# Performance work log

Hardware: AMD Instinct MI355X
Metric: run time of the kernel (lower is better)

The kernel has to match this reference:

```python
import jax, jax.numpy as jnp
import numpy as np

N_FEAT = 32
P = 3            # patch_size
K = 4            # top-k
DS = (3, 5, 7)   # displacement windows for (l3, l2, l1)
T = 3            # n_frames
EPS = 1e-12      # F.normalize eps


def _unfold(x, ksz):
    # F.unfold(x, ksz, padding=ksz//2, stride=1): [b,c,h,w] -> [b,c,ksz*ksz,h,w]
    b, c, h, w = x.shape
    pad = ksz // 2
    xp = jnp.pad(x, ((0, 0), (0, 0), (pad, pad), (pad, pad)))
    pats = [xp[:, :, i:i + h, j:j + w] for i in range(ksz) for j in range(ksz)]
    return jnp.stack(pats, axis=2)


def _agg_unit(feat_t, feat_tm1, d, agg_w, agg_b, wp_w, wp_b):
    b, c, h, w = feat_t.shape
    p2 = P * P
    ft_u = _unfold(feat_t, P).reshape(b, c * p2, h, w)        # [b,cp2,h,w]
    ftm_u = _unfold(feat_tm1, P).reshape(b, c * p2, h, w)     # [b,cp2,h,w]
    disp = jnp.transpose(_unfold(ftm_u, d), (0, 1, 3, 4, 2))  # [b,cp2,h,w,d2]
    # cosine similarity over channel*patch dim
    ft_n = ft_u / jnp.maximum(jnp.linalg.norm(ft_u, axis=1, keepdims=True), EPS)
    disp_norm = jnp.maximum(jnp.linalg.norm(disp, axis=1), EPS)          # [b,h,w,d2]
    sim = jnp.einsum('bchw,bchwd->bhwd', ft_n, disp) / disp_norm          # [b,h,w,d2]
    _, idx = jax.lax.top_k(sim, K)                                        # [b,h,w,K]
    gath = jnp.take_along_axis(disp, idx[:, None], axis=-1)               # [b,cp2,h,w,K]
    g = gath.reshape(b, c, p2, h, w, K)
    # aggregator: Conv2d(K,1,1) == weighted sum over K + scalar bias
    aggd = jnp.einsum('bcphwk,k->bcphw', g, agg_w) + agg_b                # [b,c,p2,h,w]
    aggd = jnp.transpose(aggd, (0, 1, 3, 4, 2))                           # [b,c,h,w,p2]
    # w_proj: Conv2d(2c, c*p2, 1)
    wm = jnp.einsum('oi,bihw->bohw', wp_w, jnp.concatenate([feat_t, feat_tm1], axis=1))
    wm = wm + wp_b[None, :, None, None]
    wm = jnp.transpose(wm.reshape(b, c, p2, h, w), (0, 1, 3, 4, 2))       # [b,c,h,w,p2]
    return jnp.sum(aggd * wm, axis=-1)                                    # [b,c,h,w]


def _up2(x):
    # bilinear x2, align_corners=False (half-pixel == jax.image 'linear')
    b, c, h, w = x.shape
    return jax.image.resize(x, (b, c, 2 * h, 2 * w), method='linear')


def _pixel_shuffle(x, r):
    b, c, h, w = x.shape
    co = c // (r * r)
    x = x.reshape(b, co, r, r, h, w)
    return jnp.transpose(x, (0, 1, 4, 2, 5, 3)).reshape(b, co, h * r, w * r)


def setup_inputs() -> dict:
    key = jax.random.key(0)
    ks = jax.random.split(key, 20)
    B, C, H = 1, N_FEAT, 48
    p2 = P * P
    d = {}
    d['feats_l1'] = jax.random.normal(ks[0], (B, C, T, H, H), jnp.float32)
    d['feats_l2'] = jax.random.normal(ks[1], (B, C, T, H // 2, H // 2), jnp.float32)
    d['feats_l3'] = jax.random.normal(ks[2], (B, C, T, H // 4, H // 4), jnp.float32)
    for i, name in enumerate(['l3', 'l2', 'l1']):
        d['agg_' + name + '_w'] = jax.random.normal(ks[3 + 4 * i], (K,), jnp.float32) * 0.1
        d['agg_' + name + '_b'] = jax.random.normal(ks[4 + 4 * i], (), jnp.float32) * 0.1
        d['wp_' + name + '_w'] = jax.random.normal(ks[5 + 4 * i], (C * p2, 2 * C), jnp.float32) * 0.05
        d['wp_' + name + '_b'] = jnp.zeros((C * p2,), jnp.float32)
    d['up_w'] = jax.random.normal(ks[16], (4 * C, C * T), jnp.float32) * 0.05
    d['up_b'] = jnp.zeros((4 * C,), jnp.float32)
    return d


def reference(feats_l1, feats_l2, feats_l3,
              agg_l3_w, agg_l3_b, wp_l3_w, wp_l3_b,
              agg_l2_w, agg_l2_b, wp_l2_w, wp_l2_b,
              agg_l1_w, agg_l1_b, wp_l1_w, wp_l1_b,
              up_w, up_b):
    center = T // 2
    c1 = feats_l1[:, :, center]
    c2 = feats_l2[:, :, center]
    c3 = feats_l3[:, :, center]
    a3 = [_up2(_agg_unit(c3, feats_l3[:, :, t], DS[0], agg_l3_w, agg_l3_b, wp_l3_w, wp_l3_b))
          for t in range(T)]
    a2 = [_up2(_agg_unit(c2 + a3[t], feats_l2[:, :, t] + a3[t], DS[1], agg_l2_w, agg_l2_b, wp_l2_w, wp_l2_b))
          for t in range(T)]
    a1 = [_agg_unit(c1 + a2[t], feats_l1[:, :, t] + a2[t], DS[2], agg_l1_w, agg_l1_b, wp_l1_w, wp_l1_b)
          for t in range(T)]
    x = jnp.concatenate(a1, axis=1)                                       # [b, c*T, h, w]
    x = jnp.einsum('oi,bihw->bohw', up_w, x) + up_b[None, :, None, None]  # [b, 4c, h, w]
    return _pixel_shuffle(x, 2)                                           # [b, c, 2h, 2w]
```

## Files before the change

### kernel.cpp

```cpp
#include <hip/hip_runtime.h>
#include <math.h>


template<int D, int TS>
__global__ __launch_bounds__(256, 4)
void agg_tile(const float* __restrict__ feats,
              const float* __restrict__ add,
              const float* __restrict__ agg_w,
              const float* __restrict__ agg_b,
              const float* __restrict__ wp_w,
              const float* __restrict__ wp_b,
              float* __restrict__ out,
              int H, int W, int TPW)
{
    constexpr int PD = D / 2;
    constexpr int M  = PD + 1;
    constexpr int R  = TS + 2 * M;
    constexpr int S  = TS + 2;
    constexpr int D2 = D * D;
    constexpr int NP = TS * TS;
    constexpr int NX = S * S * D2;
    constexpr int NSIM = NP * D2;
    constexpr int CS = 36;
    constexpr int USZ = (NP * 288 > NX + NSIM) ? NP * 288 : NX + NSIM;

    __shared__ float sA[R * R * CS];
    __shared__ float sC[S * S * CS];
    __shared__ float t2[R * R];
    __shared__ float s2[S * S];
    __shared__ float U[USZ];
    __shared__ int   sIdx[NP * 4];

    float* Xarr = U;
    float* sSim = U + NX;

    const int tid  = threadIdx.x;
    const int tile = blockIdx.x;
    const int t    = blockIdx.y;
    const int y0 = (tile / TPW) * TS;
    const int x0 = (tile % TPW) * TS;

    const float* addT = add ? (add + (size_t)t * 32 * H * W) : nullptr;

    for (int e = tid; e < R * R * 32; e += 256) {
        int rx = e % R, ry = (e / R) % R, c = e / (R * R);
        int yy = y0 - M + ry, xx = x0 - M + rx;
        float v = 0.f;
        if (yy >= 0 && yy < H && xx >= 0 && xx < W) {
            v = feats[((c * 3 + t) * H + yy) * W + xx];
            if (addT) v += addT[(c * H + yy) * W + xx];
        }
        sA[(ry * R + rx) * CS + c] = v;
    }
    for (int e = tid; e < S * S * 32; e += 256) {
        int rx = e % S, ry = (e / S) % S, c = e / (S * S);
        int yy = y0 - 1 + ry, xx = x0 - 1 + rx;
        float v = 0.f;
        if (yy >= 0 && yy < H && xx >= 0 && xx < W) {
            v = feats[((c * 3 + 1) * H + yy) * W + xx];
            if (addT) v += addT[(c * H + yy) * W + xx];
        }
        sC[(ry * S + rx) * CS + c] = v;
    }
    __syncthreads();

    if (tid < S * S * D) {
        const int u  = tid / D;
        const int di = tid % D;
        const int uy = u / S, ux = u % S;
        float4 cv[8];
        const float4* c4 = (const float4*)(sC + u * CS);
        #pragma unroll
        for (int i = 0; i < 8; ++i) cv[i] = c4[i];
        const float* arow = sA + ((uy + di) * R + ux) * CS;
        #pragma unroll
        for (int dj = 0; dj < D; ++dj) {
            const float4* a4 = (const float4*)(arow + dj * CS);
            float s = 0.f;
            #pragma unroll
            for (int i = 0; i < 8; ++i) {
                float4 av = a4[i];
                s += cv[i].x * av.x + cv[i].y * av.y + cv[i].z * av.z + cv[i].w * av.w;
            }
            Xarr[u * D2 + di * D + dj] = s;
        }
    }
    for (int e = tid; e < R * R; e += 256) {
        const float4* a4 = (const float4*)(sA + e * CS);
        float s = 0.f;
        #pragma unroll
        for (int cc = 0; cc < 8; ++cc) {
            float4 v = a4[cc];
            s += v.x * v.x + v.y * v.y + v.z * v.z + v.w * v.w;
        }
        t2[e] = s;
    }
    for (int e = tid; e < S * S; e += 256) {
        const float4* c4 = (const float4*)(sC + e * CS);
        float s = 0.f;
        #pragma unroll
        for (int cc = 0; cc < 8; ++cc) {
            float4 v = c4[cc];
            s += v.x * v.x + v.y * v.y + v.z * v.z + v.w * v.w;
        }
        s2[e] = s;
    }
    __syncthreads();

    for (int e = tid; e < NSIM; e += 256) {
        int p = e / D2, dd = e % D2;
        int py = p / TS, px = p % TS;
        int di = dd / D, dj = dd % D;
        int Yc = y0 + py + di - PD, Xc = x0 + px + dj - PD;
        float sim = 0.f;
        if (Yc >= 0 && Yc < H && Xc >= 0 && Xc < W) {
            float dot = 0.f, n2 = 0.f, nf = 0.f;
            #pragma unroll
            for (int qi = 0; qi < 3; ++qi)
            #pragma unroll
            for (int qj = 0; qj < 3; ++qj) {
                dot += Xarr[((py + qi) * S + (px + qj)) * D2 + dd];
                n2  += t2[(py + qi + di) * R + (px + qj + dj)];
                nf  += s2[(py + qi) * S + (px + qj)];
            }
            sim = dot / fmaxf(sqrtf(nf), 1e-12f) / fmaxf(sqrtf(n2), 1e-12f);
        }
        sSim[e] = sim;
    }
    __syncthreads();

    if (tid < NP) {
        float v0 = -3.0e38f, v1 = -3.0e38f, v2 = -3.0e38f, v3 = -3.0e38f;
        int   i0 = 0, i1 = 0, i2 = 0, i3 = 0;
        for (int dd = 0; dd < D2; ++dd) {
            float v = sSim[tid * D2 + dd];
            if (v > v0)      { v3=v2;i3=i2; v2=v1;i2=i1; v1=v0;i1=i0; v0=v;i0=dd; }
            else if (v > v1) { v3=v2;i3=i2; v2=v1;i2=i1; v1=v;i1=dd; }
            else if (v > v2) { v3=v2;i3=i2; v2=v;i2=dd; }
            else if (v > v3) { v3=v;i3=dd; }
        }
        int py = tid / TS, px = tid % TS;
        int ids[4] = {i0, i1, i2, i3};
        #pragma unroll
        for (int k = 0; k < 4; ++k) {
            int dd = ids[k];
            int di = dd / D, dj = dd % D;
            int Yc = y0 + py + di - PD, Xc = x0 + px + dj - PD;
            sIdx[tid * 4 + k] = (Yc >= 0 && Yc < H && Xc >= 0 && Xc < W) ? dd : -1;
        }
    }
    __syncthreads();

    const float4* wp4 = (const float4*)wp_w;
    for (int o = tid; o < 288; o += 256) {
        float4 w[8];
        #pragma unroll
        for (int i = 0; i < 8; ++i) w[i] = wp4[o * 16 + i];
        const float wb = wp_b[o];
        #pragma unroll 1
        for (int p = 0; p < NP; ++p) {
            int py = p / TS, px = p % TS;
            const float4* pv4 = (const float4*)(sC + ((py + 1) * S + (px + 1)) * CS);
            float acc = wb;
            #pragma unroll
            for (int i = 0; i < 8; ++i) {
                float4 pv = pv4[i];
                acc += w[i].x * pv.x + w[i].y * pv.y + w[i].z * pv.z + w[i].w * pv.w;
            }
            U[p * 288 + o] = acc;
        }
    }
    const float aw0 = agg_w[0], aw1 = agg_w[1], aw2 = agg_w[2], aw3 = agg_w[3];
    const float ab  = agg_b[0];
    for (int o = tid; o < 288; o += 256) {
        int c = o / 9, q = o % 9, qi = q / 3, qj = q % 3;
        float4 w[8];
        #pragma unroll
        for (int i = 0; i < 8; ++i) w[i] = wp4[o * 16 + 8 + i];
        #pragma unroll 1
        for (int p = 0; p < NP; ++p) {
            int py = p / TS, px = p % TS;
            const float4* pv4 = (const float4*)(sA + ((py + M) * R + (px + M)) * CS);
            float acc = U[p * 288 + o];
            #pragma unroll
            for (int i = 0; i < 8; ++i) {
                float4 pv = pv4[i];
                acc += w[i].x * pv.x + w[i].y * pv.y + w[i].z * pv.z + w[i].w * pv.w;
            }
            float aggd = ab;
            #pragma unroll
            for (int k = 0; k < 4; ++k) {
                int dd = sIdx[p * 4 + k];
                if (dd >= 0) {
                    int di = dd / D, dj = dd % D;
                    float val = sA[((py + qi + di) * R + (px + qj + dj)) * CS + c];
                    float aw = (k == 0) ? aw0 : (k == 1) ? aw1 : (k == 2) ? aw2 : aw3;
                    aggd += aw * val;
                }
            }
            U[p * 288 + o] = aggd * acc;
        }
    }
    __syncthreads();

    for (int e = tid; e < 32 * NP; e += 256) {
        int c = e / NP, p = e % NP;
        int py = p / TS, px = p % TS;
        float s = 0.f;
        #pragma unroll
        for (int q = 0; q < 9; ++q) s += U[p * 288 + c * 9 + q];
        out[((t * 32 + c) * H + (y0 + py)) * W + (x0 + px)] = s;
    }
}

__global__ void up2_kernel(const float* __restrict__ in, float* __restrict__ out,
                           int C, int h, int w)
{
    int idx = blockIdx.x * blockDim.x + threadIdx.x;
    int H = 2 * h, W = 2 * w;
    int total = C * H * W;
    if (idx >= total) return;
    int ox = idx % W;
    int oy = (idx / W) % H;
    int c  = idx / (W * H);

    int my = oy >> 1, mx = ox >> 1;
    int y0, y1, x0, x1;
    float wy0, wy1, wx0, wx1;
    if ((oy & 1) == 0) { y0 = max(my - 1, 0); y1 = my; wy0 = 0.25f; wy1 = 0.75f; }
    else               { y0 = my; y1 = min(my + 1, h - 1); wy0 = 0.75f; wy1 = 0.25f; }
    if ((ox & 1) == 0) { x0 = max(mx - 1, 0); x1 = mx; wx0 = 0.25f; wx1 = 0.75f; }
    else               { x0 = mx; x1 = min(mx + 1, w - 1); wx0 = 0.75f; wx1 = 0.25f; }

    const float* pc = in + (size_t)c * h * w;
    float v = wy0 * (wx0 * pc[y0 * w + x0] + wx1 * pc[y0 * w + x1])
            + wy1 * (wx0 * pc[y1 * w + x0] + wx1 * pc[y1 * w + x1]);
    out[idx] = v;
}

__global__ __launch_bounds__(256)
void final_kernel(const float* __restrict__ a1,
                  const float* __restrict__ up_w,
                  const float* __restrict__ up_b,
                  float* __restrict__ out)
{
    const int pix = blockIdx.x * 256 + threadIdx.x;
    const int o   = blockIdx.y;
    const int x = pix % 48, y = pix / 48;

    const float* w = up_w + o * 96;
    float acc = up_b[o];
    #pragma unroll 4
    for (int i = 0; i < 96; ++i) acc += w[i] * a1[i * 2304 + pix];

    int co = o >> 2, ry = (o >> 1) & 1, rx = o & 1;
    out[((co * 96 + 2 * y + ry) * 96) + 2 * x + rx] = acc;
}

extern "C" void kernel_launch(void* const* d_in, const int* in_sizes, int n_in,
                              void* d_out, int out_size, void* d_ws, size_t ws_size,
                              hipStream_t stream)
{
    const float* feats_l1 = (const float*)d_in[0];
    const float* feats_l2 = (const float*)d_in[1];
    const float* feats_l3 = (const float*)d_in[2];
    const float* agg_l3_w = (const float*)d_in[3];
    const float* agg_l3_b = (const float*)d_in[4];
    const float* wp_l3_w  = (const float*)d_in[5];
    const float* wp_l3_b  = (const float*)d_in[6];
    const float* agg_l2_w = (const float*)d_in[7];
    const float* agg_l2_b = (const float*)d_in[8];
    const float* wp_l2_w  = (const float*)d_in[9];
    const float* wp_l2_b  = (const float*)d_in[10];
    const float* agg_l1_w = (const float*)d_in[11];
    const float* agg_l1_b = (const float*)d_in[12];
    const float* wp_l1_w  = (const float*)d_in[13];
    const float* wp_l1_b  = (const float*)d_in[14];
    const float* up_w     = (const float*)d_in[15];
    const float* up_b     = (const float*)d_in[16];
    float* out = (float*)d_out;

    float* ws   = (float*)d_ws;
    float* agg3 = ws;
    float* a3up = agg3 + 13824;
    float* agg2 = a3up + 55296;
    float* a2up = agg2 + 55296;
    float* a1   = a2up + 221184;

    agg_tile<3, 1><<<dim3(144, 3), 256, 0, stream>>>(
        feats_l3, nullptr, agg_l3_w, agg_l3_b, wp_l3_w, wp_l3_b, agg3, 12, 12, 12);
    up2_kernel<<<(96 * 24 * 24 + 255) / 256, 256, 0, stream>>>(agg3, a3up, 96, 12, 12);

    agg_tile<5, 2><<<dim3(144, 3), 256, 0, stream>>>(
        feats_l2, a3up, agg_l2_w, agg_l2_b, wp_l2_w, wp_l2_b, agg2, 24, 24, 12);
    up2_kernel<<<(96 * 48 * 48 + 255) / 256, 256, 0, stream>>>(agg2, a2up, 96, 24, 24);

    agg_tile<7, 3><<<dim3(256, 3), 256, 0, stream>>>(
        feats_l1, a2up, agg_l1_w, agg_l1_b, wp_l1_w, wp_l1_b, a1, 48, 48, 16);

    final_kernel<<<dim3(9, 128), 256, 0, stream>>>(a1, up_w, up_b, out);
}
```

Baseline: 171.4 us.

## Fuse bilinear upsample into aggregation tile loads and shrink tiles for occupancy

Removes the two separate up2 kernels and instead computes the bilinear x2 upsample on the fly while loading the halo tiles in agg_tile, which drops two launches and two intermediate buffers. Tile sizes for levels 2 and 1 are reduced (TS 2→1, 3→2) with more blocks, and launch bounds are raised to 8 waves per SIMD. The similarity loop is rewritten to stride over all S²·D² work items with a cached center vector. The trade-off is redundant bilinear work per halo pixel and more halo overlap across smaller tiles.

```diff
diff --git a/kernel.cpp b/kernel.cpp
--- a/kernel.cpp
+++ b/kernel.cpp
@@ -2,8 +2,22 @@
 #include <math.h>
 
 
-template<int D, int TS>
-__global__ __launch_bounds__(256, 4)
+__device__ __forceinline__ float up2s(const float* __restrict__ src,
+                                      int h, int w, int oy, int ox)
+{
+    int my = oy >> 1, mx = ox >> 1;
+    int y0, y1, x0, x1;
+    float wy0, wy1, wx0, wx1;
+    if ((oy & 1) == 0) { y0 = max(my - 1, 0); y1 = my; wy0 = 0.25f; wy1 = 0.75f; }
+    else               { y0 = my; y1 = min(my + 1, h - 1); wy0 = 0.75f; wy1 = 0.25f; }
+    if ((ox & 1) == 0) { x0 = max(mx - 1, 0); x1 = mx; wx0 = 0.25f; wx1 = 0.75f; }
+    else               { x0 = mx; x1 = min(mx + 1, w - 1); wx0 = 0.75f; wx1 = 0.25f; }
+    return wy0 * (wx0 * src[y0 * w + x0] + wx1 * src[y0 * w + x1])
+         + wy1 * (wx0 * src[y1 * w + x0] + wx1 * src[y1 * w + x1]);
+}
+
+template<int D, int TS, bool HA>
+__global__ __launch_bounds__(256, 8)
 void agg_tile(const float* __restrict__ feats,
               const float* __restrict__ add,
               const float* __restrict__ agg_w,
@@ -11,18 +25,20 @@
               const float* __restrict__ wp_w,
               const float* __restrict__ wp_b,
               float* __restrict__ out,
-              int H, int W, int TPW)
+              int H, int W, int TPW, int ah, int aw_)
 {
     constexpr int PD = D / 2;
     constexpr int M  = PD + 1;
     constexpr int R  = TS + 2 * M;
     constexpr int S  = TS + 2;
+    constexpr int S2 = S * S;
     constexpr int D2 = D * D;
     constexpr int NP = TS * TS;
-    constexpr int NX = S * S * D2;
+    constexpr int NX = S2 * D2;
     constexpr int NSIM = NP * D2;
     constexpr int CS = 36;
     constexpr int USZ = (NP * 288 > NX + NSIM) ? NP * 288 : NX + NSIM;
+    static_assert(NX <= 256 || 256 % S2 == 0, "u-invariance needs 256%S2==0");
 
     __shared__ float sA[R * R * CS];
     __shared__ float sC[S * S * CS];
@@ -40,7 +56,7 @@
     const int y0 = (tile / TPW) * TS;
     const int x0 = (tile % TPW) * TS;
 
-    const float* addT = add ? (add + (size_t)t * 32 * H * W) : nullptr;
+    const float* addT = HA ? (add + (size_t)t * 32 * ah * aw_) : nullptr;
 
     for (int e = tid; e < R * R * 32; e += 256) {
         int rx = e % R, ry = (e / R) % R, c = e / (R * R);
@@ -48,7 +64,7 @@
         float v = 0.f;
         if (yy >= 0 && yy < H && xx >= 0 && xx < W) {
             v = feats[((c * 3 + t) * H + yy) * W + xx];
-            if (addT) v += addT[(c * H + yy) * W + xx];
+            if (HA) v += up2s(addT + c * ah * aw_, ah, aw_, yy, xx);
         }
         sA[(ry * R + rx) * CS + c] = v;
     }
@@ -58,31 +74,33 @@
         float v = 0.f;
         if (yy >= 0 && yy < H && xx >= 0 && xx < W) {
             v = feats[((c * 3 + 1) * H + yy) * W + xx];
-            if (addT) v += addT[(c * H + yy) * W + xx];
+            if (HA) v += up2s(addT + c * ah * aw_, ah, aw_, yy, xx);
         }
         sC[(ry * S + rx) * CS + c] = v;
     }
     __syncthreads();
 
-    if (tid < S * S * D) {
-        const int u  = tid / D;
-        const int di = tid % D;
-        const int uy = u / S, ux = u % S;
+    {
         float4 cv[8];
-        const float4* c4 = (const float4*)(sC + u * CS);
-        #pragma unroll
-        for (int i = 0; i < 8; ++i) cv[i] = c4[i];
-        const float* arow = sA + ((uy + di) * R + ux) * CS;
-        #pragma unroll
-        for (int dj = 0; dj < D; ++dj) {
-            const float4* a4 = (const float4*)(arow + dj * CS);
+        int ulast = -1;
+        for (int e = tid; e < NX; e += 256) {
+            const int u = e % S2, dd = e / S2;
+            if (u != ulast) {
+                const float4* c4 = (const float4*)(sC + u * CS);
+                #pragma unroll
+                for (int i = 0; i < 8; ++i) cv[i] = c4[i];
+                ulast = u;
+            }
+            const int uy = u / S, ux = u % S;
+            const int di = dd / D, dj = dd % D;
+            const float4* a4 = (const float4*)(sA + ((uy + di) * R + (ux + dj)) * CS);
             float s = 0.f;
             #pragma unroll
             for (int i = 0; i < 8; ++i) {
                 float4 av = a4[i];
                 s += cv[i].x * av.x + cv[i].y * av.y + cv[i].z * av.z + cv[i].w * av.w;
             }
-            Xarr[u * D2 + di * D + dj] = s;
+            Xarr[u * D2 + dd] = s;
         }
     }
     for (int e = tid; e < R * R; e += 256) {
@@ -211,31 +229,6 @@
         for (int q = 0; q < 9; ++q) s += U[p * 288 + c * 9 + q];
         out[((t * 32 + c) * H + (y0 + py)) * W + (x0 + px)] = s;
     }
-}
-
-__global__ void up2_kernel(const float* __restrict__ in, float* __restrict__ out,
-                           int C, int h, int w)
-{
-    int idx = blockIdx.x * blockDim.x + threadIdx.x;
-    int H = 2 * h, W = 2 * w;
-    int total = C * H * W;
-    if (idx >= total) return;
-    int ox = idx % W;
-    int oy = (idx / W) % H;
-    int c  = idx / (W * H);
-
-    int my = oy >> 1, mx = ox >> 1;
-    int y0, y1, x0, x1;
-    float wy0, wy1, wx0, wx1;
-    if ((oy & 1) == 0) { y0 = max(my - 1, 0); y1 = my; wy0 = 0.25f; wy1 = 0.75f; }
-    else               { y0 = my; y1 = min(my + 1, h - 1); wy0 = 0.75f; wy1 = 0.25f; }
-    if ((ox & 1) == 0) { x0 = max(mx - 1, 0); x1 = mx; wx0 = 0.25f; wx1 = 0.75f; }
-    else               { x0 = mx; x1 = min(mx + 1, w - 1); wx0 = 0.75f; wx1 = 0.25f; }
-
-    const float* pc = in + (size_t)c * h * w;
-    float v = wy0 * (wx0 * pc[y0 * w + x0] + wx1 * pc[y0 * w + x1])
-            + wy1 * (wx0 * pc[y1 * w + x0] + wx1 * pc[y1 * w + x1]);
-    out[idx] = v;
 }
 
 __global__ __launch_bounds__(256)
@@ -282,21 +275,20 @@
 
     float* ws   = (float*)d_ws;
     float* agg3 = ws;
-    float* a3up = agg3 + 13824;
-    float* agg2 = a3up + 55296;
-    float* a2up = agg2 + 55296;
-    float* a1   = a2up + 221184;
-
-    agg_tile<3, 1><<<dim3(144, 3), 256, 0, stream>>>(
-        feats_l3, nullptr, agg_l3_w, agg_l3_b, wp_l3_w, wp_l3_b, agg3, 12, 12, 12);
-    up2_kernel<<<(96 * 24 * 24 + 255) / 256, 256, 0, stream>>>(agg3, a3up, 96, 12, 12);
-
-    agg_tile<5, 2><<<dim3(144, 3), 256, 0, stream>>>(
-        feats_l2, a3up, agg_l2_w, agg_l2_b, wp_l2_w, wp_l2_b, agg2, 24, 24, 12);
-    up2_kernel<<<(96 * 48 * 48 + 255) / 256, 256, 0, stream>>>(agg2, a2up, 96, 24, 24);
-
-    agg_tile<7, 3><<<dim3(256, 3), 256, 0, stream>>>(
-        feats_l1, a2up, agg_l1_w, agg_l1_b, wp_l1_w, wp_l1_b, a1, 48, 48, 16);
+    float* agg2 = agg3 + 13824;
+    float* a1   = agg2 + 55296;
+
+    agg_tile<3, 1, false><<<dim3(144, 3), 256, 0, stream>>>(
+        feats_l3, nullptr, agg_l3_w, agg_l3_b, wp_l3_w, wp_l3_b, agg3,
+        12, 12, 12, 0, 0);
+
+    agg_tile<5, 1, true><<<dim3(576, 3), 256, 0, stream>>>(
+        feats_l2, agg3, agg_l2_w, agg_l2_b, wp_l2_w, wp_l2_b, agg2,
+        24, 24, 24, 12, 12);
+
+    agg_tile<7, 2, true><<<dim3(576, 3), 256, 0, stream>>>(
+        feats_l1, agg2, agg_l1_w, agg_l1_b, wp_l1_w, wp_l1_b, a1,
+        48, 48, 24, 24, 24);
 
     final_kernel<<<dim3(9, 128), 256, 0, stream>>>(a1, up_w, up_b, out);
 }
```

New measurement: 201.2 us. 17.3% more time.
